# Kernel tuning notes

Hardware: AMD Instinct MI355X
Metric: run time of the kernel (lower is better)

Reference implementation:

```python
import jax, jax.numpy as jnp
import numpy as np

B, S, D = 2, 2048, 2048
H, KVH = 32, 8
HD = D // H            # 64
G = H // KVH           # 4 kv groups
SCALE = 1.0 / np.sqrt(HD)


def setup_inputs() -> dict:
    key = jax.random.key(0)
    k1, k2, k3, k4, k5 = jax.random.split(key, 5)
    hidden_states = jax.random.normal(k1, (B, S, D), dtype=jnp.float32)
    Wq = jax.random.normal(k2, (D, H * HD), dtype=jnp.float32) * 0.02
    Wk = jax.random.normal(k3, (D, KVH * HD), dtype=jnp.float32) * 0.02
    Wv = jax.random.normal(k4, (D, KVH * HD), dtype=jnp.float32) * 0.02
    Wo = jax.random.normal(k5, (H * HD, D), dtype=jnp.float32) * 0.02
    return {"hidden_states": hidden_states, "Wq": Wq, "Wk": Wk, "Wv": Wv, "Wo": Wo}


def reference(hidden_states, Wq, Wk, Wv, Wo):
    B_, S_, _ = hidden_states.shape
    q = (hidden_states @ Wq).reshape(B_, S_, H, HD).transpose(0, 2, 1, 3)      # [B,H,S,HD]
    k = (hidden_states @ Wk).reshape(B_, S_, KVH, HD).transpose(0, 2, 1, 3)    # [B,KVH,S,HD]
    v = (hidden_states @ Wv).reshape(B_, S_, KVH, HD).transpose(0, 2, 1, 3)
    # repeat_interleave over head dim: kv head g serves q heads [g*G, (g+1)*G)
    k = jnp.repeat(k, G, axis=1)  # [B,H,S,HD]
    v = jnp.repeat(v, G, axis=1)
    scores = jnp.einsum('bhqd,bhkd->bhqk', q, k) * SCALE
    probs = jax.nn.softmax(scores.astype(jnp.float32), axis=-1).astype(q.dtype)
    # dropout is identity in eval mode
    out = jnp.einsum('bhqk,bhkd->bhqd', probs, v)             # [B,H,S,HD]
    out = out.transpose(0, 2, 1, 3).reshape(B_, S_, H * HD)   # [B,S,D]
    return out @ Wo
```

## Files before the change

kernel.cpp:

```cpp
#include <hip/hip_runtime.h>
#include <hip/hip_bf16.h>

typedef unsigned short u16;
typedef __attribute__((ext_vector_type(8))) short short8;
typedef __attribute__((ext_vector_type(4))) float f32x4;
typedef __attribute__((ext_vector_type(4))) unsigned short u16x4;

#define S_LEN 2048
#define NH 32
#define NKV 8
#define QSCALE 0.18033688011112042f
#define PSHIFT 14.0f

__device__ __forceinline__ float fexp2(float x) { return __builtin_amdgcn_exp2f(x); }

__device__ __forceinline__ u16 f2bf(float f) {
  unsigned int u = __builtin_bit_cast(unsigned int, f);
  u += 0x7fffu + ((u >> 16) & 1u);
  return (u16)(u >> 16);
}

__device__ __forceinline__ unsigned int pk2bf(float a, float b) {
  float2 t; t.x = a; t.y = b;
  __hip_bfloat162 h = __float22bfloat162_rn(t);
  unsigned int r;
  __builtin_memcpy(&r, &h, 4);
  return r;
}

__device__ __forceinline__ void async16(const void* g, void* l) {
  __builtin_amdgcn_global_load_lds(
      (__attribute__((address_space(1))) void*)g,
      (__attribute__((address_space(3))) void*)l, 16, 0, 0);
}

__global__ __launch_bounds__(256) void prep_kernel(const float* __restrict__ X,
                                                   const float* __restrict__ Wq,
                                                   const float* __restrict__ Wk,
                                                   const float* __restrict__ Wv,
                                                   const float* __restrict__ Wo,
                                                   u16* __restrict__ Xb,
                                                   u16* __restrict__ Wqt,
                                                   u16* __restrict__ Wkt,
                                                   u16* __restrict__ Wvt,
                                                   u16* __restrict__ Wot) {
  __shared__ float tile[32][33];
  int bx = blockIdx.x, tid = threadIdx.x;
  if (bx < 8192) {
    int idx = bx * 256 + tid;
    float4 v = ((const float4*)X)[idx];
    u16x4 o;
    o.x = f2bf(v.x); o.y = f2bf(v.y); o.z = f2bf(v.z); o.w = f2bf(v.w);
    *(u16x4*)&Xb[(size_t)idx * 4] = o;
    return;
  }
  const float* in; u16* out; int N, bi;
  if (bx < 12288)      { bi = bx - 8192;  in = Wq; out = Wqt; N = 2048; }
  else if (bx < 13312) { bi = bx - 12288; in = Wk; out = Wkt; N = 512; }
  else if (bx < 14336) { bi = bx - 13312; in = Wv; out = Wvt; N = 512; }
  else                 { bi = bx - 14336; in = Wo; out = Wot; N = 2048; }
  const int K = 2048;
  int nbx = N >> 5;
  int n0 = (bi % nbx) * 32, k0 = (bi / nbx) * 32;
  int tx = tid & 31, ty = tid >> 5;
#pragma unroll
  for (int i = 0; i < 32; i += 8)
    tile[ty + i][tx] = in[(size_t)(k0 + ty + i) * N + n0 + tx];
  __syncthreads();
#pragma unroll
  for (int i = 0; i < 32; i += 8)
    out[(size_t)(n0 + ty + i) * K + k0 + tx] = f2bf(tile[tx][ty + i]);
}

__global__ __launch_bounds__(256) void gemm_qkv(const u16* __restrict__ A,
                                                const u16* __restrict__ Wqt,
                                                const u16* __restrict__ Wkvt,
                                                u16* __restrict__ Qb,
                                                u16* __restrict__ KVb) {
  __shared__ u16 lds_a[128 * 32];
  __shared__ u16 lds_b[128 * 32];
  int tid = threadIdx.x, bx = blockIdx.x;
  int mode, bm, bn;
  const u16* Bt;
  if (bx < 512) { mode = 0; bm = bx >> 4; bn = bx & 15; Bt = Wqt; }
  else          { mode = 1; int b2 = bx - 512; bm = b2 >> 3; bn = b2 & 7; Bt = Wkvt; }
  const int K = 2048;
  int w = tid >> 6, lane = tid & 63, qd = lane >> 4, ln = lane & 15;
  int wm = w >> 1, wn = w & 1;
  const f32x4 z4 = {0.f, 0.f, 0.f, 0.f};
  f32x4 acc[4][4];
#pragma unroll
  for (int i = 0; i < 4; ++i)
#pragma unroll
    for (int j = 0; j < 4; ++j) acc[i][j] = z4;

  const u16* Ab = A + (size_t)bm * 128 * K;
  const u16* Bb = Bt + (size_t)bn * 128 * K;
  int row0 = tid >> 2, c0 = tid & 3;
  int g0 = c0 ^ (row0 & 3) ^ ((row0 >> 2) & 3);
  int s1 = tid + 256, row1 = s1 >> 2, c1 = s1 & 3;
  int g1 = c1 ^ (row1 & 3) ^ ((row1 >> 2) & 3);
  int pat = (ln & 3) ^ ((ln >> 2) & 3);
  int goff = (qd ^ pat) * 8;

  for (int kt = 0; kt < K; kt += 32) {
    async16(Ab + (size_t)row0 * K + kt + g0 * 8, &lds_a[tid * 8]);
    async16(Ab + (size_t)row1 * K + kt + g1 * 8, &lds_a[2048 + tid * 8]);
    async16(Bb + (size_t)row0 * K + kt + g0 * 8, &lds_b[tid * 8]);
    async16(Bb + (size_t)row1 * K + kt + g1 * 8, &lds_b[2048 + tid * 8]);
    __syncthreads();
    short8 af[4], bf[4];
#pragma unroll
    for (int i = 0; i < 4; ++i)
      af[i] = *(const short8*)&lds_a[(wm * 64 + i * 16 + ln) * 32 + goff];
#pragma unroll
    for (int j = 0; j < 4; ++j)
      bf[j] = *(const short8*)&lds_b[(wn * 64 + j * 16 + ln) * 32 + goff];
#pragma unroll
    for (int i = 0; i < 4; ++i)
#pragma unroll
      for (int j = 0; j < 4; ++j)
        acc[i][j] = __builtin_amdgcn_mfma_f32_16x16x32_bf16(af[i], bf[j], acc[i][j], 0, 0, 0);
    __syncthreads();
  }

#pragma unroll
  for (int i = 0; i < 4; ++i)
#pragma unroll
    for (int r = 0; r < 4; ++r) {
      int m = bm * 128 + wm * 64 + i * 16 + qd * 4 + r;
      int b = m >> 11, s = m & 2047;
#pragma unroll
      for (int j = 0; j < 4; ++j) {
        int n = bn * 128 + wn * 64 + j * 16 + ln;
        float v = acc[i][j][r];
        int hh = n >> 6, hd = n & 63;
        if (mode == 0) {
          Qb[(((size_t)(b * NH + hh)) * S_LEN + s) * 64 + hd] = f2bf(v * QSCALE);
        } else {
          if (hh < 8)
            KVb[(((size_t)(b * NKV + hh)) * S_LEN + s) * 64 + hd] = f2bf(v);
          else
            KVb[2097152 + (((size_t)(b * NKV + (hh - 8))) * 64 + hd) * S_LEN + s] = f2bf(v);
        }
      }
    }
}

__global__ __launch_bounds__(256) void gemm_out(const u16* __restrict__ A,
                                                const u16* __restrict__ Bt,
                                                float* __restrict__ outp) {
  __shared__ u16 lds_a[128 * 32];
  __shared__ u16 lds_b[128 * 32];
  const int K = 2048, N = 2048;
  int tid = threadIdx.x;
  int bm = blockIdx.x >> 4, bn = blockIdx.x & 15;
  int w = tid >> 6, lane = tid & 63, qd = lane >> 4, ln = lane & 15;
  int wm = w >> 1, wn = w & 1;
  const f32x4 z4 = {0.f, 0.f, 0.f, 0.f};
  f32x4 acc[4][4];
#pragma unroll
  for (int i = 0; i < 4; ++i)
#pragma unroll
    for (int j = 0; j < 4; ++j) acc[i][j] = z4;

  const u16* Ab = A + (size_t)bm * 128 * K;
  const u16* Bb = Bt + (size_t)bn * 128 * K;
  int row0 = tid >> 2, c0 = tid & 3;
  int g0 = c0 ^ (row0 & 3) ^ ((row0 >> 2) & 3);
  int s1 = tid + 256, row1 = s1 >> 2, c1 = s1 & 3;
  int g1 = c1 ^ (row1 & 3) ^ ((row1 >> 2) & 3);
  int pat = (ln & 3) ^ ((ln >> 2) & 3);
  int goff = (qd ^ pat) * 8;

  for (int kt = 0; kt < K; kt += 32) {
    async16(Ab + (size_t)row0 * K + kt + g0 * 8, &lds_a[tid * 8]);
    async16(Ab + (size_t)row1 * K + kt + g1 * 8, &lds_a[2048 + tid * 8]);
    async16(Bb + (size_t)row0 * K + kt + g0 * 8, &lds_b[tid * 8]);
    async16(Bb + (size_t)row1 * K + kt + g1 * 8, &lds_b[2048 + tid * 8]);
    __syncthreads();
    short8 af[4], bf[4];
#pragma unroll
    for (int i = 0; i < 4; ++i)
      af[i] = *(const short8*)&lds_a[(wm * 64 + i * 16 + ln) * 32 + goff];
#pragma unroll
    for (int j = 0; j < 4; ++j)
      bf[j] = *(const short8*)&lds_b[(wn * 64 + j * 16 + ln) * 32 + goff];
#pragma unroll
    for (int i = 0; i < 4; ++i)
#pragma unroll
      for (int j = 0; j < 4; ++j)
        acc[i][j] = __builtin_amdgcn_mfma_f32_16x16x32_bf16(af[i], bf[j], acc[i][j], 0, 0, 0);
    __syncthreads();
  }

#pragma unroll
  for (int i = 0; i < 4; ++i)
#pragma unroll
    for (int r = 0; r < 4; ++r) {
      int m = bm * 128 + wm * 64 + i * 16 + qd * 4 + r;
#pragma unroll
      for (int j = 0; j < 4; ++j) {
        int n = bn * 128 + wn * 64 + j * 16 + ln;
        outp[(size_t)m * N + n] = acc[i][j][r];
      }
    }
}

__global__ __launch_bounds__(256) void attn_kernel(const u16* __restrict__ Q,
                                                   const u16* __restrict__ K,
                                                   const u16* __restrict__ VT,
                                                   u16* __restrict__ Ao) {
  __shared__ u16 lds_k[8192];
  __shared__ u16 lds_v[8192];
  __shared__ u16 lds_p[4096];
  int tid = threadIdx.x;
  int w = tid >> 6, lane = tid & 63, qd = lane >> 4, ln = lane & 15;
  int qt = blockIdx.x & 15, bh = blockIdx.x >> 4;
  int b = bh >> 5, h = bh & 31, g = h >> 2;
  const u16* gQ = Q + ((size_t)bh * S_LEN + qt * 128) * 64;
  const u16* gK = K + (size_t)(b * NKV + g) * S_LEN * 64;
  const u16* gV = VT + (size_t)(b * NKV + g) * 64 * S_LEN;

  int pat7 = ln & 7;
  int sQ = (ln >> 1) & 3;
  int pw = w * 1024;

#pragma unroll
  for (int k = 0; k < 4; ++k) {
    int s = tid + k * 256;
    int q = s >> 3, c = s & 7, gg = c ^ (q & 7);
    async16(gQ + (size_t)q * 64 + gg * 8, &lds_k[s * 8]);
  }
  __syncthreads();
  short8 qf[2][2];
#pragma unroll
  for (int i = 0; i < 2; ++i)
#pragma unroll
    for (int kc = 0; kc < 2; ++kc)
      qf[i][kc] = *(const short8*)&lds_k[(w * 32 + i * 16 + ln) * 64 +
                                         ((kc * 4 + qd) ^ pat7) * 8];
  __syncthreads();

  const f32x4 psh4 = {-PSHIFT, -PSHIFT, -PSHIFT, -PSHIFT};
  f32x4 accO[2][4];
  float li[2] = {0.f, 0.f};
#pragma unroll
  for (int i = 0; i < 2; ++i)
#pragma unroll
    for (int jn = 0; jn < 4; ++jn) accO[i][jn] = {0.f, 0.f, 0.f, 0.f};

  for (int kt = 0; kt < 16; ++kt) {
#pragma unroll
    for (int k = 0; k < 4; ++k) {
      int s = tid + k * 256;
      int kv = s >> 3, c = s & 7, gg = c ^ (kv & 7);
      async16(gK + (size_t)(kt * 128 + kv) * 64 + gg * 8, &lds_k[s * 8]);
    }
#pragma unroll
    for (int k = 0; k < 4; ++k) {
      int s = tid + k * 256;
      int hd = s >> 4, c = s & 15, gg = c ^ (hd & 7);
      async16(gV + (size_t)hd * S_LEN + kt * 128 + gg * 8, &lds_v[s * 8]);
    }
    __syncthreads();

    f32x4 sc[2][8];
    __builtin_amdgcn_s_setprio(1);
#pragma unroll
    for (int j = 0; j < 8; ++j) {
      short8 kf0 = *(const short8*)&lds_k[(j * 16 + ln) * 64 + ((0 + qd) ^ pat7) * 8];
      short8 kf1 = *(const short8*)&lds_k[(j * 16 + ln) * 64 + ((4 + qd) ^ pat7) * 8];
#pragma unroll
      for (int i = 0; i < 2; ++i) {
        sc[i][j] = __builtin_amdgcn_mfma_f32_16x16x32_bf16(kf0, qf[i][0], psh4, 0, 0, 0);
        sc[i][j] = __builtin_amdgcn_mfma_f32_16x16x32_bf16(kf1, qf[i][1], sc[i][j], 0, 0, 0);
      }
    }
    __builtin_amdgcn_s_setprio(0);

#pragma unroll
    for (int ph = 0; ph < 4; ++ph) {
#pragma unroll
      for (int i = 0; i < 2; ++i)
#pragma unroll
        for (int jj = 0; jj < 2; ++jj) {
          int j = ph * 2 + jj;
          float p0 = fexp2(sc[i][j][0]);
          float p1 = fexp2(sc[i][j][1]);
          float p2 = fexp2(sc[i][j][2]);
          float p3 = fexp2(sc[i][j][3]);
          li[i] += (p0 + p1) + (p2 + p3);
          uint2 pk;
          pk.x = pk2bf(p0, p1);
          pk.y = pk2bf(p2, p3);
          int pg = jj * 2 + (qd >> 1);
          *(uint2*)&lds_p[pw + (i * 16 + ln) * 32 + ((pg ^ sQ) * 8 + (qd & 1) * 4)] = pk;
        }
      short8 pf0 = *(const short8*)&lds_p[pw + ln * 32 + (qd ^ sQ) * 8];
      short8 pf1 = *(const short8*)&lds_p[pw + (16 + ln) * 32 + (qd ^ sQ) * 8];
      __builtin_amdgcn_s_setprio(1);
#pragma unroll
      for (int jn = 0; jn < 4; ++jn) {
        short8 vf = *(const short8*)&lds_v[(jn * 16 + ln) * 128 +
                                           (((ph * 4 + qd) ^ pat7) * 8)];
        accO[0][jn] = __builtin_amdgcn_mfma_f32_16x16x32_bf16(vf, pf0, accO[0][jn], 0, 0, 0);
        accO[1][jn] = __builtin_amdgcn_mfma_f32_16x16x32_bf16(vf, pf1, accO[1][jn], 0, 0, 0);
      }
      __builtin_amdgcn_s_setprio(0);
    }
    __syncthreads();
  }

#pragma unroll
  for (int i = 0; i < 2; ++i) {
    float l = li[i];
    l += __shfl_xor(l, 16);
    l += __shfl_xor(l, 32);
    float inv = 1.f / l;
    int q = qt * 128 + w * 32 + i * 16 + ln;
    size_t base = ((size_t)b * S_LEN + q) * 2048 + h * 64;
#pragma unroll
    for (int jn = 0; jn < 4; ++jn) {
      u16x4 o;
#pragma unroll
      for (int r = 0; r < 4; ++r) o[r] = f2bf(accO[i][jn][r] * inv);
      *(u16x4*)&Ao[base + jn * 16 + qd * 4] = o;
    }
  }
}

extern "C" void kernel_launch(void* const* d_in, const int* in_sizes, int n_in,
                              void* d_out, int out_size, void* d_ws, size_t ws_size,
                              hipStream_t stream) {
  const float* X  = (const float*)d_in[0];
  const float* Wq = (const float*)d_in[1];
  const float* Wk = (const float*)d_in[2];
  const float* Wv = (const float*)d_in[3];
  const float* Wo = (const float*)d_in[4];
  char* ws = (char*)d_ws;
  u16* Xb  = (u16*)(ws);
  u16* Wqt = (u16*)(ws + 16777216);
  u16* Wkt = (u16*)(ws + 25165824);
  u16* Wvt = (u16*)(ws + 27262976);
  u16* Wot = (u16*)(ws + 29360128);
  u16* Qb  = (u16*)(ws + 37748736);
  u16* Kb  = (u16*)(ws + 54525952);
  u16* VTb = (u16*)(ws + 58720256);
  u16* Ab  = (u16*)(ws + 62914560);
  float* out = (float*)d_out;

  prep_kernel<<<18432, 256, 0, stream>>>(X, Wq, Wk, Wv, Wo, Xb, Wqt, Wkt, Wvt, Wot);
  gemm_qkv<<<768, 256, 0, stream>>>(Xb, Wqt, Wkt, Qb, Kb);
  attn_kernel<<<1024, 256, 0, stream>>>(Qb, Kb, VTb, Ab);
  gemm_out<<<512, 256, 0, stream>>>(Ab, Wot, out);
}
```

Measured before the change: 327.7 us.

## Double-buffer K/V tiles in 64-key chunks to overlap loads with compute

```diff
diff --git a/kernel.cpp b/kernel.cpp
--- a/kernel.cpp
+++ b/kernel.cpp
@@ -211,8 +211,8 @@
                                                    const u16* __restrict__ K,
                                                    const u16* __restrict__ VT,
                                                    u16* __restrict__ Ao) {
-  __shared__ u16 lds_k[8192];
-  __shared__ u16 lds_v[8192];
+  __shared__ u16 lds_k[2][4096];
+  __shared__ u16 lds_v[2][4096];
   __shared__ u16 lds_p[4096];
   int tid = threadIdx.x;
   int w = tid >> 6, lane = tid & 63, qd = lane >> 4, ln = lane & 15;
@@ -226,11 +226,15 @@
   int sQ = (ln >> 1) & 3;
   int pw = w * 1024;
 
+  int s0 = tid, r0 = s0 >> 3, c0 = s0 & 7, gg0 = c0 ^ (r0 & 7);
+  int s1 = tid + 256, r1 = s1 >> 3, c1 = s1 & 7, gg1 = c1 ^ (r1 & 7);
+
+  u16* qstage = &lds_k[0][0];
 #pragma unroll
   for (int k = 0; k < 4; ++k) {
     int s = tid + k * 256;
     int q = s >> 3, c = s & 7, gg = c ^ (q & 7);
-    async16(gQ + (size_t)q * 64 + gg * 8, &lds_k[s * 8]);
+    async16(gQ + (size_t)q * 64 + gg * 8, &qstage[s * 8]);
   }
   __syncthreads();
   short8 qf[2][2];
@@ -238,8 +242,14 @@
   for (int i = 0; i < 2; ++i)
 #pragma unroll
     for (int kc = 0; kc < 2; ++kc)
-      qf[i][kc] = *(const short8*)&lds_k[(w * 32 + i * 16 + ln) * 64 +
-                                         ((kc * 4 + qd) ^ pat7) * 8];
+      qf[i][kc] = *(const short8*)&qstage[(w * 32 + i * 16 + ln) * 64 +
+                                          ((kc * 4 + qd) ^ pat7) * 8];
+  __syncthreads();
+
+  async16(gK + (size_t)(r0)*64 + gg0 * 8, &lds_k[0][s0 * 8]);
+  async16(gK + (size_t)(r1)*64 + gg1 * 8, &lds_k[0][s1 * 8]);
+  async16(gV + (size_t)r0 * S_LEN + gg0 * 8, &lds_v[0][s0 * 8]);
+  async16(gV + (size_t)r1 * S_LEN + gg1 * 8, &lds_v[0][s1 * 8]);
   __syncthreads();
 
   const f32x4 psh4 = {-PSHIFT, -PSHIFT, -PSHIFT, -PSHIFT};
@@ -250,27 +260,24 @@
 #pragma unroll
     for (int jn = 0; jn < 4; ++jn) accO[i][jn] = {0.f, 0.f, 0.f, 0.f};
 
-  for (int kt = 0; kt < 16; ++kt) {
-#pragma unroll
-    for (int k = 0; k < 4; ++k) {
-      int s = tid + k * 256;
-      int kv = s >> 3, c = s & 7, gg = c ^ (kv & 7);
-      async16(gK + (size_t)(kt * 128 + kv) * 64 + gg * 8, &lds_k[s * 8]);
-    }
-#pragma unroll
-    for (int k = 0; k < 4; ++k) {
-      int s = tid + k * 256;
-      int hd = s >> 4, c = s & 15, gg = c ^ (hd & 7);
-      async16(gV + (size_t)hd * S_LEN + kt * 128 + gg * 8, &lds_v[s * 8]);
-    }
-    __syncthreads();
-
-    f32x4 sc[2][8];
+  for (int c = 0; c < 32; ++c) {
+    int cur = c & 1;
+    if (c < 31) {
+      int nb = cur ^ 1, cn = c + 1;
+      async16(gK + (size_t)(cn * 64 + r0) * 64 + gg0 * 8, &lds_k[nb][s0 * 8]);
+      async16(gK + (size_t)(cn * 64 + r1) * 64 + gg1 * 8, &lds_k[nb][s1 * 8]);
+      async16(gV + (size_t)r0 * S_LEN + cn * 64 + gg0 * 8, &lds_v[nb][s0 * 8]);
+      async16(gV + (size_t)r1 * S_LEN + cn * 64 + gg1 * 8, &lds_v[nb][s1 * 8]);
+    }
+    const u16* kb = lds_k[cur];
+    const u16* vb = lds_v[cur];
+
+    f32x4 sc[2][4];
     __builtin_amdgcn_s_setprio(1);
 #pragma unroll
-    for (int j = 0; j < 8; ++j) {
-      short8 kf0 = *(const short8*)&lds_k[(j * 16 + ln) * 64 + ((0 + qd) ^ pat7) * 8];
-      short8 kf1 = *(const short8*)&lds_k[(j * 16 + ln) * 64 + ((4 + qd) ^ pat7) * 8];
+    for (int j = 0; j < 4; ++j) {
+      short8 kf0 = *(const short8*)&kb[(j * 16 + ln) * 64 + ((0 + qd) ^ pat7) * 8];
+      short8 kf1 = *(const short8*)&kb[(j * 16 + ln) * 64 + ((4 + qd) ^ pat7) * 8];
 #pragma unroll
       for (int i = 0; i < 2; ++i) {
         sc[i][j] = __builtin_amdgcn_mfma_f32_16x16x32_bf16(kf0, qf[i][0], psh4, 0, 0, 0);
@@ -280,7 +287,7 @@
     __builtin_amdgcn_s_setprio(0);
 
 #pragma unroll
-    for (int ph = 0; ph < 4; ++ph) {
+    for (int ph = 0; ph < 2; ++ph) {
 #pragma unroll
       for (int i = 0; i < 2; ++i)
 #pragma unroll
@@ -302,8 +309,8 @@
       __builtin_amdgcn_s_setprio(1);
 #pragma unroll
       for (int jn = 0; jn < 4; ++jn) {
-        short8 vf = *(const short8*)&lds_v[(jn * 16 + ln) * 128 +
-                                           (((ph * 4 + qd) ^ pat7) * 8)];
+        short8 vf = *(const short8*)&vb[(jn * 16 + ln) * 64 +
+                                        (((ph * 4 + qd) ^ pat7) * 8)];
         accO[0][jn] = __builtin_amdgcn_mfma_f32_16x16x32_bf16(vf, pf0, accO[0][jn], 0, 0, 0);
         accO[1][jn] = __builtin_amdgcn_mfma_f32_16x16x32_bf16(vf, pf1, accO[1][jn], 0, 0, 0);
       }
```

New measurement: 331.4 us. No clear change (+1.1%).
